# Performance work log

Measured on AMD Instinct MI355X. Metric: run time of the kernel, lower is better.

Reference implementation:

```python
import jax, jax.numpy as jnp
import numpy as np

B, L, D, H = 2, 2048, 1024, 16
HD = D // H


def setup_inputs() -> dict:
    key = jax.random.key(0)
    ks = jax.random.split(key, 14)
    s = 0.02
    return {
        "hidden_states": jax.random.normal(ks[0], (B, L, D), jnp.float32),
        "position_embeddings": jax.random.normal(ks[1], (B, L, D), jnp.float32),
        "Wcq": jax.random.normal(ks[2], (D, D), jnp.float32) * s,
        "bcq": jnp.zeros((D,), jnp.float32),
        "Wck": jax.random.normal(ks[3], (D, D), jnp.float32) * s,
        "bck": jnp.zeros((D,), jnp.float32),
        "Wpq": jax.random.normal(ks[4], (D, D), jnp.float32) * s,
        "bpq": jnp.zeros((D,), jnp.float32),
        "Wpk": jax.random.normal(ks[5], (D, D), jnp.float32) * s,
        "bpk": jnp.zeros((D,), jnp.float32),
        "rel_bias": jnp.zeros((1, H, 1, 1), jnp.float32),
        "Wo": jax.random.normal(ks[6], (D, D), jnp.float32) * s,
        "bo": jnp.zeros((D,), jnp.float32),
    }


def _split_heads(x):
    # [B, L, D] -> [B, H, L, HD]
    b, l, _ = x.shape
    return x.reshape(b, l, H, HD).transpose(0, 2, 1, 3)


def reference(hidden_states, position_embeddings, Wcq, bcq, Wck, bck,
              Wpq, bpq, Wpk, bpk, rel_bias, Wo, bo):
    cq = _split_heads(hidden_states @ Wcq + bcq)
    ck = _split_heads(hidden_states @ Wck + bck)
    # NOTE: original code (faithfully reproduced) uses content_key as the value
    cv = ck
    pq = _split_heads(position_embeddings @ Wpq + bpq)
    pk = _split_heads(position_embeddings @ Wpk + bpk)

    scores = (jnp.einsum("bhqd,bhkd->bhqk", cq, ck)
              + jnp.einsum("bhqd,bhkd->bhqk", pq, pk)
              + rel_bias)
    attn_weights = jax.nn.softmax(scores / jnp.sqrt(jnp.float32(HD)), axis=-1)
    ctx = jnp.einsum("bhqk,bhkd->bhqd", attn_weights, cv)
    ctx = ctx.transpose(0, 2, 1, 3).reshape(hidden_states.shape[0], -1, D)
    output = ctx @ Wo + bo
    return output, attn_weights
```

## Files before the change

kernel.cpp:

```cpp
#include <hip/hip_runtime.h>
#include <hip/hip_bf16.h>
#include <math.h>


#define Bc 2
#define Lc 2048
#define Dc 1024
#define Hc 16
#define Mc (Bc*Lc)
#define NT 32

typedef __attribute__((ext_vector_type(8))) __bf16 bf16x8;
typedef __attribute__((ext_vector_type(4))) float f32x4;
typedef __attribute__((ext_vector_type(16))) float f32x16;
typedef __attribute__((ext_vector_type(2))) unsigned u32x2;

union U4 { unsigned u[4]; bf16x8 v; };

__device__ __forceinline__ void gl_lds16(const void* g, void* l) {
    __builtin_amdgcn_global_load_lds(
        (const __attribute__((address_space(1))) void*)g,
        (__attribute__((address_space(3))) void*)l, 16, 0, 0);
}
__device__ __forceinline__ unsigned pkbf(float a, float b) {
    unsigned short ua = __builtin_bit_cast(unsigned short, (__bf16)a);
    unsigned short ub = __builtin_bit_cast(unsigned short, (__bf16)b);
    return (unsigned)ua | ((unsigned)ub << 16);
}
__device__ __forceinline__ float lo2f(unsigned u){ return __builtin_bit_cast(float, u << 16); }
__device__ __forceinline__ float hi2f(unsigned u){ return __builtin_bit_cast(float, u & 0xffff0000u); }
#define E2(x) __builtin_amdgcn_exp2f(x)

#define WAIT_VM0  asm volatile("s_waitcnt vmcnt(0)" ::: "memory")
#define WAIT_VM4  asm volatile("s_waitcnt vmcnt(4)" ::: "memory")
#define WAIT_VM8  asm volatile("s_waitcnt vmcnt(8)" ::: "memory")
#define WAIT_VM12 asm volatile("s_waitcnt vmcnt(12)" ::: "memory")
#define WAIT_LG0  asm volatile("s_waitcnt lgkmcnt(0)" ::: "memory")
#define SBAR __builtin_amdgcn_sched_barrier(0)
#define BARRIER do { __builtin_amdgcn_sched_barrier(0); __builtin_amdgcn_s_barrier(); __builtin_amdgcn_sched_barrier(0); } while (0)

__global__ __launch_bounds__(256) void prep_kernel(
    const float* __restrict__ hidden, const float* __restrict__ pos,
    const float* __restrict__ Wcq, const float* __restrict__ Wck,
    const float* __restrict__ Wpq, const float* __restrict__ Wpk,
    const float* __restrict__ Wo,
    __bf16* __restrict__ Wt, __bf16* __restrict__ Woh, __bf16* __restrict__ Wol,
    __bf16* __restrict__ Xh, __bf16* __restrict__ Xp)
{
    const int z = blockIdx.z;
    const int t = threadIdx.x;
    if (z >= 5) {
        const float* X = (z==5) ? hidden : pos;
        __bf16* dst    = (z==5) ? Xh : Xp;
        const size_t base = ((size_t)(blockIdx.y*16 + blockIdx.x)*256 + t) * 128;
        #pragma unroll
        for (int c = 0; c < 16; ++c) {
            const float* sp = X + base + c*8;
            float4 v0 = *(const float4*)sp;
            float4 v1 = *(const float4*)(sp + 4);
            bf16x8 o;
            o[0]=(__bf16)v0.x; o[1]=(__bf16)v0.y; o[2]=(__bf16)v0.z; o[3]=(__bf16)v0.w;
            o[4]=(__bf16)v1.x; o[5]=(__bf16)v1.y; o[6]=(__bf16)v1.z; o[7]=(__bf16)v1.w;
            *(bf16x8*)(dst + base + c*8) = o;
        }
        return;
    }
    const float* W = (z==0)?Wcq:(z==1)?Wck:(z==2)?Wpq:(z==3)?Wpk:Wo;
    const int n  = blockIdx.x*64 + (t & 63);
    const int k0 = blockIdx.y*128 + (t >> 6)*32;
    float v[32];
    #pragma unroll
    for (int j = 0; j < 32; ++j) v[j] = W[(size_t)(k0+j)*Dc + n];
    if (z < 4) {
        __bf16* dst = Wt + (size_t)z*Dc*Dc + (size_t)n*Dc + k0;
        #pragma unroll
        for (int c = 0; c < 4; ++c) {
            bf16x8 o;
            #pragma unroll
            for (int j = 0; j < 8; ++j) o[j] = (__bf16)v[c*8+j];
            *(bf16x8*)(dst + c*8) = o;
        }
    } else {
        __bf16* dh = Woh + (size_t)n*Dc + k0;
        __bf16* dl = Wol + (size_t)n*Dc + k0;
        #pragma unroll
        for (int c = 0; c < 4; ++c) {
            bf16x8 oh, ol;
            #pragma unroll
            for (int j = 0; j < 8; ++j) {
                float x = v[c*8+j];
                __bf16 hi = (__bf16)x;
                oh[j] = hi; ol[j] = (__bf16)(x - (float)hi);
            }
            *(bf16x8*)(dh + c*8) = oh;
            *(bf16x8*)(dl + c*8) = ol;
        }
    }
}

__global__ __launch_bounds__(256) void proj_kernel(
    const __bf16* __restrict__ Xh, const __bf16* __restrict__ Xp,
    const __bf16* __restrict__ Wt,
    const float* __restrict__ bcq, const float* __restrict__ bck,
    const float* __restrict__ bpq, const float* __restrict__ bpk,
    __bf16* __restrict__ Qc, __bf16* __restrict__ Kc)
{
    const int g = blockIdx.x;
    const int nblk = g >> 7, sg = g & 127, mblk = sg & 31, z = sg >> 5;
    const int m0 = mblk*128, n0 = nblk*128;
    const __bf16* X = (z < 2) ? Xh : Xp;
    const __bf16* Wz = Wt + (size_t)z*Dc*Dc;
    const float* bias = (z==0)?bcq:(z==1)?bck:(z==2)?bpq:bpk;
    __bf16* dst = (z & 1) ? Kc : Qc;
    const int half = z >> 1;
    const float scale = (z & 1) ? 1.0f : 0.18033688011112042f;

    const int t = threadIdx.x, lane = t & 63, w = t >> 6;
    const int wm = w >> 1, wn = w & 1;

    __shared__ __align__(16) __bf16 As[128][32];
    __shared__ __align__(16) __bf16 Bs[128][32];

    const int brow4 = lane >> 2;
    const int bcol  = ((lane & 3) ^ (brow4 & 3)) * 8;

    f32x4 acc[4][4] = {};

    for (int k0 = 0; k0 < Dc; k0 += 32) {
        #pragma unroll
        for (int i = 0; i < 2; ++i) {
            int row = 16*(2*w+i) + brow4;
            gl_lds16(X  + (size_t)(m0+row)*Dc + k0 + bcol, (char*)As + (2*w+i)*1024);
            gl_lds16(Wz + (size_t)(n0+row)*Dc + k0 + bcol, (char*)Bs + (2*w+i)*1024);
        }
        WAIT_VM0; __syncthreads();
        bf16x8 a[4], b[4];
        const int s2 = lane >> 4;
        #pragma unroll
        for (int i = 0; i < 4; ++i) {
            int Ra = wm*64 + i*16 + (lane&15);
            int Rb = wn*64 + i*16 + (lane&15);
            a[i] = *(const bf16x8*)((const char*)&As[Ra][0] + ((s2 ^ (Ra&3))*16));
            b[i] = *(const bf16x8*)((const char*)&Bs[Rb][0] + ((s2 ^ (Rb&3))*16));
        }
        #pragma unroll
        for (int mi = 0; mi < 4; ++mi)
            #pragma unroll
            for (int ni = 0; ni < 4; ++ni)
                acc[mi][ni] = __builtin_amdgcn_mfma_f32_16x16x32_bf16(a[mi], b[ni], acc[mi][ni], 0, 0, 0);
        __syncthreads();
    }
    #pragma unroll
    for (int mi = 0; mi < 4; ++mi)
        #pragma unroll
        for (int ni = 0; ni < 4; ++ni)
            #pragma unroll
            for (int r = 0; r < 4; ++r) {
                int row = m0 + wm*64 + mi*16 + (lane>>4)*4 + r;
                int col = n0 + wn*64 + ni*16 + (lane&15);
                float v = (acc[mi][ni][r] + bias[col]) * scale;
                int bb = row >> 11, l = row & (Lc-1);
                int hh = col >> 6,  hd = col & 63;
                dst[(((size_t)bb*Hc + hh)*Lc + l)*128 + half*64 + hd] = (__bf16)v;
            }
}

__global__ __launch_bounds__(256) void vt_kernel(
    const __bf16* __restrict__ Kc, __bf16* __restrict__ VT)
{
    const int l0 = blockIdx.x * 128, hb = blockIdx.y;
    const int t = threadIdx.x, w = t >> 6, lane = t & 63;
    __shared__ __bf16 T[128][72];
    const __bf16* src = Kc + ((size_t)hb*Lc + l0)*128;
    {
        const int lr = t >> 3, cc = t & 7;
        #pragma unroll
        for (int j = 0; j < 4; ++j)
            *(bf16x8*)&T[lr + j*32][cc*8] = *(const bf16x8*)(src + (size_t)(lr + j*32)*128 + cc*8);
    }
    __syncthreads();
    {
        const int d = lane;
        __bf16* dstp = VT + ((size_t)hb*64 + d)*Lc + l0 + w*32;
        #pragma unroll
        for (int j = 0; j < 4; ++j) {
            bf16x8 o;
            #pragma unroll
            for (int i = 0; i < 8; ++i) o[i] = T[w*32 + j*8 + i][d];
            *(bf16x8*)(dstp + j*8) = o;
        }
    }
}

__global__ __launch_bounds__(256, 3) void attn1_kernel(
    const __bf16* __restrict__ Qc, const __bf16* __restrict__ Kc,
    const float* __restrict__ rel_bias, float* __restrict__ baddp)
{
    const int g = blockIdx.x;
    const int qt = g >> 5, hb = g & 31, h = hb & 15;
    const int q0 = qt * 128;
    const int t = threadIdx.x, lane = t & 63, w = t >> 6;
    const int ln31 = lane & 31, hi = lane >> 5;

    const __bf16* Qp = Qc + (size_t)hb * Lc * 128;
    const __bf16* Kp = Kc + (size_t)hb * Lc * 128;

    __shared__ __align__(16) char smem[49152];

    bf16x8 qa[8];
    {
        const __bf16* qrow = Qp + (size_t)(q0 + w*32 + ln31) * 128 + hi*8;
        #pragma unroll
        for (int ks = 0; ks < 8; ++ks) qa[ks] = *(const bf16x8*)(qrow + ks*16);
    }

    int kof[4];
    #pragma unroll
    for (int c = 0; c < 4; ++c) {
        int rl = c*4 + (lane >> 4);
        int rr = w*16 + rl;
        kof[c] = rr*128 + (((lane & 15) ^ rl) * 8);
    }
    int kR[8];
    #pragma unroll
    for (int ks = 0; ks < 8; ++ks) kR[ks] = ((ks*2 + hi) ^ (lane & 15)) * 8;

    #define STAGE_K(B, KT) do { \
        const __bf16* kb_ = Kp + (size_t)(KT)*8192; \
        gl_lds16(kb_ + kof[0], smem + ((B)*64 + w*16 +  0)*256); \
        gl_lds16(kb_ + kof[1], smem + ((B)*64 + w*16 +  4)*256); \
        gl_lds16(kb_ + kof[2], smem + ((B)*64 + w*16 +  8)*256); \
        gl_lds16(kb_ + kof[3], smem + ((B)*64 + w*16 + 12)*256); \
    } while (0)
    #define KB(B, ROW, KS) (*(const bf16x8*)(smem + ((B)*64 + (ROW))*256 + kR[KS]*2))

    const float bc = rel_bias[h] * 0.18033688011112042f;
    float lp[4] = {0.f, 0.f, 0.f, 0.f};

    STAGE_K(0, 0); STAGE_K(1, 1);
    WAIT_VM4; BARRIER;
    for (int kt = 0; kt < NT; ++kt) {
        if (kt+2 < NT) STAGE_K((kt+2) % 3, kt+2);
        SBAR;
        const int buf = kt % 3;
        f32x16 s0, s1;
        #pragma unroll
        for (int r = 0; r < 16; ++r) { s0[r] = bc; s1[r] = bc; }
        __builtin_amdgcn_s_setprio(1);
        #pragma unroll
        for (int ks = 0; ks < 8; ++ks) {
            bf16x8 kb0 = KB(buf, ln31, ks);
            bf16x8 kb1 = KB(buf, 32 + ln31, ks);
            s0 = __builtin_amdgcn_mfma_f32_32x32x16_bf16(kb0, qa[ks], s0, 0, 0, 0);
            s1 = __builtin_amdgcn_mfma_f32_32x32x16_bf16(kb1, qa[ks], s1, 0, 0, 0);
        }
        __builtin_amdgcn_s_setprio(0);
        #pragma unroll
        for (int r = 0; r < 16; ++r) {
            lp[r & 3] += E2(s0[r]);
            lp[r & 3] += E2(s1[r]);
        }
        if (kt+2 < NT) { WAIT_VM4; } else { WAIT_VM0; }
        BARRIER;
    }
    float lsum = (lp[0] + lp[1]) + (lp[2] + lp[3]);
    lsum += __shfl_xor(lsum, 32);
    if (!hi) baddp[(size_t)hb*Lc + q0 + w*32 + ln31] = bc - log2f(lsum);
    #undef STAGE_K
    #undef KB
}

__global__ __launch_bounds__(256, 2) void attn2_kernel(
    const __bf16* __restrict__ Qc, const __bf16* __restrict__ Kc,
    const __bf16* __restrict__ VT, const float* __restrict__ baddp,
    float* __restrict__ attn, __bf16* __restrict__ ctxh)
{
    const int g = blockIdx.x;
    const int qt = g >> 5, hb = g & 31, h = hb & 15, bb = hb >> 4;
    const int q0 = qt * 128;
    const int t = threadIdx.x, lane = t & 63, w = t >> 6;
    const int ln31 = lane & 31, hi = lane >> 5;

    const __bf16* Qp = Qc + (size_t)hb * Lc * 128;
    const __bf16* Kp = Kc + (size_t)hb * Lc * 128;
    const __bf16* Vp = VT + (size_t)hb * 64 * Lc;

    __shared__ __align__(16) char smem[81920];
    char* const VsB = smem + 49152;
    char* const PsW = smem + 65536 + w*4096;

    bf16x8 qa[8];
    {
        const __bf16* qrow = Qp + (size_t)(q0 + w*32 + ln31) * 128 + hi*8;
        #pragma unroll
        for (int ks = 0; ks < 8; ++ks) qa[ks] = *(const bf16x8*)(qrow + ks*16);
    }
    const float badd = baddp[(size_t)hb*Lc + q0 + w*32 + ln31];

    int kof[4];
    #pragma unroll
    for (int c = 0; c < 4; ++c) {
        int rl = c*4 + (lane >> 4);
        int rr = w*16 + rl;
        kof[c] = rr*128 + (((lane & 15) ^ rl) * 8);
    }
    int vof[2];
    #pragma unroll
    for (int c = 0; c < 2; ++c) {
        int dl = lane >> 3;
        int dd = w*16 + c*8 + dl;
        vof[c] = dd*2048 + (((lane & 7) ^ dl) * 8);
    }
    int kR[8];
    #pragma unroll
    for (int ks = 0; ks < 8; ++ks) kR[ks] = ((ks*2 + hi) ^ (lane & 15)) * 8;
    int vR[4];
    #pragma unroll
    for (int ks = 0; ks < 4; ++ks) vR[ks] = ((ks*2 + hi) ^ (lane & 7)) * 8;

    #define STAGE_K(B, KT) do { \
        const __bf16* kb_ = Kp + (size_t)(KT)*8192; \
        gl_lds16(kb_ + kof[0], smem + ((B)*64 + w*16 +  0)*256); \
        gl_lds16(kb_ + kof[1], smem + ((B)*64 + w*16 +  4)*256); \
        gl_lds16(kb_ + kof[2], smem + ((B)*64 + w*16 +  8)*256); \
        gl_lds16(kb_ + kof[3], smem + ((B)*64 + w*16 + 12)*256); \
    } while (0)
    #define STAGE_V(B, KT) do { \
        const __bf16* vb_ = Vp + (KT)*64; \
        gl_lds16(vb_ + vof[0], VsB + ((B)*64 + w*16 + 0)*128); \
        gl_lds16(vb_ + vof[1], VsB + ((B)*64 + w*16 + 8)*128); \
    } while (0)
    #define KB(B, ROW, KS) (*(const bf16x8*)(smem + ((B)*64 + (ROW))*256 + kR[KS]*2))
    #define VB(B, ROW, KS) (*(const bf16x8*)(VsB  + ((B)*64 + (ROW))*128 + vR[KS]*2))

    f32x16 ctx0 = {}, ctx1 = {};
    float* abase = attn + ((size_t)hb*Lc + q0 + w*32)*Lc;
    const int rr2 = lane >> 4;
    const int s8  = lane & 15;

    STAGE_K(0, 0); STAGE_V(0, 0); STAGE_K(1, 1);
    WAIT_VM4; BARRIER;

    for (int kt = 0; kt < NT; ++kt) {
        if (kt+1 < NT) STAGE_V((kt+1) & 1, kt+1);
        if (kt+2 < NT) STAGE_K((kt+2) % 3, kt+2);
        SBAR;
        const int buf = kt % 3;
        f32x16 s0, s1;
        #pragma unroll
        for (int r = 0; r < 16; ++r) { s0[r] = badd; s1[r] = badd; }
        __builtin_amdgcn_s_setprio(1);
        #pragma unroll
        for (int ks = 0; ks < 8; ++ks) {
            bf16x8 kb0 = KB(buf, ln31, ks);
            bf16x8 kb1 = KB(buf, 32 + ln31, ks);
            s0 = __builtin_amdgcn_mfma_f32_32x32x16_bf16(kb0, qa[ks], s0, 0, 0, 0);
            s1 = __builtin_amdgcn_mfma_f32_32x32x16_bf16(kb1, qa[ks], s1, 0, 0, 0);
        }
        __builtin_amdgcn_s_setprio(0);
        unsigned u0[8], u1[8], r0[8], r1[8];
        #pragma unroll
        for (int gq = 0; gq < 4; ++gq) {
            u0[gq]   = pkbf(E2(s0[4*gq+0]), E2(s0[4*gq+1]));
            u1[gq]   = pkbf(E2(s0[4*gq+2]), E2(s0[4*gq+3]));
            u0[4+gq] = pkbf(E2(s1[4*gq+0]), E2(s1[4*gq+1]));
            u1[4+gq] = pkbf(E2(s1[4*gq+2]), E2(s1[4*gq+3]));
        }
        #pragma unroll
        for (int gq = 0; gq < 8; ++gq) {
            r0[gq] = __shfl_xor(u0[gq], 32);
            r1[gq] = __shfl_xor(u1[gq], 32);
        }
        bf16x8 pb[4];
        #pragma unroll
        for (int ks = 0; ks < 4; ++ks) {
            const int gq = 2*ks + hi;
            U4 u;
            u.u[0] = hi ? r0[gq] : u0[gq];
            u.u[1] = hi ? r1[gq] : u1[gq];
            u.u[2] = hi ? u0[gq] : r0[gq];
            u.u[3] = hi ? u1[gq] : r1[gq];
            pb[ks] = u.v;
            *(bf16x8*)(PsW + ln31*128 + ((gq ^ (ln31 & 7))*16)) = u.v;
        }
        __builtin_amdgcn_s_setprio(1);
        #pragma unroll
        for (int ks = 0; ks < 4; ++ks) {
            bf16x8 v0 = VB(kt & 1, ln31, ks);
            bf16x8 v1 = VB(kt & 1, 32 + ln31, ks);
            ctx0 = __builtin_amdgcn_mfma_f32_32x32x16_bf16(pb[ks], v0, ctx0, 0, 0, 0);
            ctx1 = __builtin_amdgcn_mfma_f32_32x32x16_bf16(pb[ks], v1, ctx1, 0, 0, 0);
        }
        __builtin_amdgcn_s_setprio(0);
        WAIT_LG0; SBAR;
        #pragma unroll
        for (int j = 0; j < 8; ++j) {
            const int row = j*4 + rr2;
            u32x2 d = *(const u32x2*)(PsW + row*128 + (((s8>>1) ^ (row&7))*16) + (s8&1)*8);
            f32x4 o;
            o[0]=lo2f(d[0]); o[1]=hi2f(d[0]); o[2]=lo2f(d[1]); o[3]=hi2f(d[1]);
            __builtin_nontemporal_store(o, (f32x4*)(abase + (size_t)row*Lc + kt*64 + s8*4));
        }
        if (kt+1 < NT) {
            if (kt+2 < NT) { WAIT_VM12; } else { WAIT_VM8; }
            BARRIER;
        }
    }

    #pragma unroll
    for (int r = 0; r < 16; ++r) {
        const int R = (r&3) + 8*(r>>2) + 4*hi;
        const size_t row = (size_t)bb*Lc + q0 + w*32 + R;
        ctxh[row*Dc + h*64 + ln31]      = (__bf16)ctx0[r];
        ctxh[row*Dc + h*64 + 32 + ln31] = (__bf16)ctx1[r];
    }
    #undef STAGE_K
    #undef STAGE_V
    #undef KB
    #undef VB
}

__global__ __launch_bounds__(256) void out_kernel(
    const __bf16* __restrict__ ctxh, const __bf16* __restrict__ Woh,
    const __bf16* __restrict__ Wol, const float* __restrict__ bo,
    float* __restrict__ out)
{
    const int m0 = blockIdx.y * 128, n0 = blockIdx.x * 128;
    const int t = threadIdx.x, lane = t & 63, w = t >> 6;
    const int wm = w >> 1, wn = w & 1;

    __shared__ __align__(16) __bf16 As[128][32];
    __shared__ __align__(16) __bf16 Bh[128][32];
    __shared__ __align__(16) __bf16 Bl[128][32];

    const int row4 = lane >> 2;
    const int scol = ((lane & 3) ^ (row4 & 3)) * 8;

    f32x4 acc[4][4] = {};

    for (int k0 = 0; k0 < Dc; k0 += 32) {
        #pragma unroll
        for (int i = 0; i < 2; ++i) {
            int row = 16*(2*w+i) + row4;
            gl_lds16(ctxh + (size_t)(m0+row)*Dc + k0 + scol, (char*)As + (2*w+i)*1024);
            gl_lds16(Woh  + (size_t)(n0+row)*Dc + k0 + scol, (char*)Bh + (2*w+i)*1024);
            gl_lds16(Wol  + (size_t)(n0+row)*Dc + k0 + scol, (char*)Bl + (2*w+i)*1024);
        }
        WAIT_VM0; __syncthreads();
        bf16x8 a[4], bh[4], bl[4];
        const int s2 = lane >> 4;
        #pragma unroll
        for (int i = 0; i < 4; ++i) {
            int Ra = wm*64 + i*16 + (lane&15);
            int Rb = wn*64 + i*16 + (lane&15);
            a[i]  = *(const bf16x8*)((const char*)&As[Ra][0] + ((s2 ^ (Ra&3))*16));
            bh[i] = *(const bf16x8*)((const char*)&Bh[Rb][0] + ((s2 ^ (Rb&3))*16));
            bl[i] = *(const bf16x8*)((const char*)&Bl[Rb][0] + ((s2 ^ (Rb&3))*16));
        }
        #pragma unroll
        for (int mi = 0; mi < 4; ++mi)
            #pragma unroll
            for (int ni = 0; ni < 4; ++ni) {
                acc[mi][ni] = __builtin_amdgcn_mfma_f32_16x16x32_bf16(a[mi], bh[ni], acc[mi][ni], 0, 0, 0);
                acc[mi][ni] = __builtin_amdgcn_mfma_f32_16x16x32_bf16(a[mi], bl[ni], acc[mi][ni], 0, 0, 0);
            }
        __syncthreads();
    }
    #pragma unroll
    for (int mi = 0; mi < 4; ++mi)
        #pragma unroll
        for (int ni = 0; ni < 4; ++ni)
            #pragma unroll
            for (int r = 0; r < 4; ++r) {
                int row = m0 + wm*64 + mi*16 + (lane>>4)*4 + r;
                int col = n0 + wn*64 + ni*16 + (lane&15);
                __builtin_nontemporal_store(acc[mi][ni][r] + bo[col],
                                            out + (size_t)row * Dc + col);
            }
}

extern "C" void kernel_launch(void* const* d_in, const int* in_sizes, int n_in,
                              void* d_out, int out_size, void* d_ws, size_t ws_size,
                              hipStream_t stream)
{
    const float* hidden = (const float*)d_in[0];
    const float* pos    = (const float*)d_in[1];
    const float* Wcq = (const float*)d_in[2];  const float* bcq = (const float*)d_in[3];
    const float* Wck = (const float*)d_in[4];  const float* bck = (const float*)d_in[5];
    const float* Wpq = (const float*)d_in[6];  const float* bpq = (const float*)d_in[7];
    const float* Wpk = (const float*)d_in[8];  const float* bpk = (const float*)d_in[9];
    const float* relb = (const float*)d_in[10];
    const float* Wo  = (const float*)d_in[11]; const float* bo  = (const float*)d_in[12];

    float* out  = (float*)d_out;
    float* attn = out + (size_t)Mc * Dc;

    __bf16* ws   = (__bf16*)d_ws;
    __bf16* Woh  = ws;
    __bf16* Wol  = ws + (1u<<20);
    __bf16* Wt   = ws + (2u<<20);
    __bf16* ctxh = Wt;
    __bf16* Qc   = ws + (6u<<20);
    __bf16* Kc   = ws + (14u<<20);
    __bf16* VTb  = ws + (22u<<20);
    float*  badd = (float*)(ws + (26u<<20));

    __bf16* Xh = (__bf16*)attn;
    __bf16* Xp = Xh + (4u<<20);

    prep_kernel<<<dim3(16, 8, 7), 256, 0, stream>>>(
        hidden, pos, Wcq, Wck, Wpq, Wpk, Wo, Wt, Woh, Wol, Xh, Xp);
    proj_kernel<<<dim3(1024), 256, 0, stream>>>(Xh, Xp, Wt, bcq, bck, bpq, bpk, Qc, Kc);
    vt_kernel<<<dim3(Lc/128, 32), 256, 0, stream>>>(Kc, VTb);
    attn1_kernel<<<dim3(512), 256, 0, stream>>>(Qc, Kc, relb, badd);
    attn2_kernel<<<dim3(512), 256, 0, stream>>>(Qc, Kc, VTb, badd, attn, ctxh);
    out_kernel<<<dim3(8, 32), 256, 0, stream>>>(ctxh, Woh, Wol, bo, out);
}
```

Before: 330.3 us.

## Triple-buffer LDS staging in projection and output GEMM kernels

The QK projection GEMM and the output GEMM move from a single shared-memory tile with a full load wait each k-step to a three-deep ring of buffers. Two stages are prefetched ahead, and partial vmcnt waits let global-to-LDS loads overlap the MFMA work. s_setprio is raised around the MFMA block so compute waves get scheduling priority. The cost is more LDS per block (48KB and 72KB), which may lower occupancy.

```diff
diff --git a/kernel.cpp b/kernel.cpp
--- a/kernel.cpp
+++ b/kernel.cpp
@@ -33,6 +33,7 @@
 
 #define WAIT_VM0  asm volatile("s_waitcnt vmcnt(0)" ::: "memory")
 #define WAIT_VM4  asm volatile("s_waitcnt vmcnt(4)" ::: "memory")
+#define WAIT_VM6  asm volatile("s_waitcnt vmcnt(6)" ::: "memory")
 #define WAIT_VM8  asm volatile("s_waitcnt vmcnt(8)" ::: "memory")
 #define WAIT_VM12 asm volatile("s_waitcnt vmcnt(12)" ::: "memory")
 #define WAIT_LG0  asm volatile("s_waitcnt lgkmcnt(0)" ::: "memory")
@@ -118,38 +119,49 @@
     const int t = threadIdx.x, lane = t & 63, w = t >> 6;
     const int wm = w >> 1, wn = w & 1;
 
-    __shared__ __align__(16) __bf16 As[128][32];
-    __shared__ __align__(16) __bf16 Bs[128][32];
+    __shared__ __align__(16) char smem[49152];
 
     const int brow4 = lane >> 2;
     const int bcol  = ((lane & 3) ^ (brow4 & 3)) * 8;
 
     f32x4 acc[4][4] = {};
 
-    for (int k0 = 0; k0 < Dc; k0 += 32) {
-        #pragma unroll
-        for (int i = 0; i < 2; ++i) {
-            int row = 16*(2*w+i) + brow4;
-            gl_lds16(X  + (size_t)(m0+row)*Dc + k0 + bcol, (char*)As + (2*w+i)*1024);
-            gl_lds16(Wz + (size_t)(n0+row)*Dc + k0 + bcol, (char*)Bs + (2*w+i)*1024);
-        }
-        WAIT_VM0; __syncthreads();
+    #define STAGE_P(B, KT) do { \
+        const int k0_ = (KT)*32; \
+        _Pragma("unroll") \
+        for (int i = 0; i < 2; ++i) { \
+            int row = 16*(2*w+i) + brow4; \
+            gl_lds16(X  + (size_t)(m0+row)*Dc + k0_ + bcol, smem + (B)*16384 + (2*w+i)*1024); \
+            gl_lds16(Wz + (size_t)(n0+row)*Dc + k0_ + bcol, smem + (B)*16384 + 8192 + (2*w+i)*1024); \
+        } \
+    } while (0)
+
+    STAGE_P(0, 0); STAGE_P(1, 1);
+    WAIT_VM4; BARRIER;
+    for (int kt = 0; kt < 32; ++kt) {
+        if (kt+2 < 32) STAGE_P((kt+2) % 3, kt+2);
+        SBAR;
+        const int buf = kt % 3;
         bf16x8 a[4], b[4];
         const int s2 = lane >> 4;
         #pragma unroll
         for (int i = 0; i < 4; ++i) {
             int Ra = wm*64 + i*16 + (lane&15);
             int Rb = wn*64 + i*16 + (lane&15);
-            a[i] = *(const bf16x8*)((const char*)&As[Ra][0] + ((s2 ^ (Ra&3))*16));
-            b[i] = *(const bf16x8*)((const char*)&Bs[Rb][0] + ((s2 ^ (Rb&3))*16));
-        }
+            a[i] = *(const bf16x8*)(smem + buf*16384 + Ra*64 + ((s2 ^ (Ra&3))*16));
+            b[i] = *(const bf16x8*)(smem + buf*16384 + 8192 + Rb*64 + ((s2 ^ (Rb&3))*16));
+        }
+        __builtin_amdgcn_s_setprio(1);
         #pragma unroll
         for (int mi = 0; mi < 4; ++mi)
             #pragma unroll
             for (int ni = 0; ni < 4; ++ni)
                 acc[mi][ni] = __builtin_amdgcn_mfma_f32_16x16x32_bf16(a[mi], b[ni], acc[mi][ni], 0, 0, 0);
-        __syncthreads();
-    }
+        __builtin_amdgcn_s_setprio(0);
+        if (kt+2 < 32) { WAIT_VM4; } else { WAIT_VM0; }
+        BARRIER;
+    }
+    #undef STAGE_P
     #pragma unroll
     for (int mi = 0; mi < 4; ++mi)
         #pragma unroll
@@ -429,34 +441,41 @@
     const int t = threadIdx.x, lane = t & 63, w = t >> 6;
     const int wm = w >> 1, wn = w & 1;
 
-    __shared__ __align__(16) __bf16 As[128][32];
-    __shared__ __align__(16) __bf16 Bh[128][32];
-    __shared__ __align__(16) __bf16 Bl[128][32];
+    __shared__ __align__(16) char smem[73728];
 
     const int row4 = lane >> 2;
     const int scol = ((lane & 3) ^ (row4 & 3)) * 8;
 
     f32x4 acc[4][4] = {};
 
-    for (int k0 = 0; k0 < Dc; k0 += 32) {
-        #pragma unroll
-        for (int i = 0; i < 2; ++i) {
-            int row = 16*(2*w+i) + row4;
-            gl_lds16(ctxh + (size_t)(m0+row)*Dc + k0 + scol, (char*)As + (2*w+i)*1024);
-            gl_lds16(Woh  + (size_t)(n0+row)*Dc + k0 + scol, (char*)Bh + (2*w+i)*1024);
-            gl_lds16(Wol  + (size_t)(n0+row)*Dc + k0 + scol, (char*)Bl + (2*w+i)*1024);
-        }
-        WAIT_VM0; __syncthreads();
+    #define STAGE_O(B, KT) do { \
+        const int k0_ = (KT)*32; \
+        _Pragma("unroll") \
+        for (int i = 0; i < 2; ++i) { \
+            int row = 16*(2*w+i) + row4; \
+            gl_lds16(ctxh + (size_t)(m0+row)*Dc + k0_ + scol, smem + (B)*24576 + (2*w+i)*1024); \
+            gl_lds16(Woh  + (size_t)(n0+row)*Dc + k0_ + scol, smem + (B)*24576 + 8192 + (2*w+i)*1024); \
+            gl_lds16(Wol  + (size_t)(n0+row)*Dc + k0_ + scol, smem + (B)*24576 + 16384 + (2*w+i)*1024); \
+        } \
+    } while (0)
+
+    STAGE_O(0, 0); STAGE_O(1, 1);
+    WAIT_VM6; BARRIER;
+    for (int kt = 0; kt < 32; ++kt) {
+        if (kt+2 < 32) STAGE_O((kt+2) % 3, kt+2);
+        SBAR;
+        const int buf = kt % 3;
         bf16x8 a[4], bh[4], bl[4];
         const int s2 = lane >> 4;
         #pragma unroll
         for (int i = 0; i < 4; ++i) {
             int Ra = wm*64 + i*16 + (lane&15);
             int Rb = wn*64 + i*16 + (lane&15);
-            a[i]  = *(const bf16x8*)((const char*)&As[Ra][0] + ((s2 ^ (Ra&3))*16));
-            bh[i] = *(const bf16x8*)((const char*)&Bh[Rb][0] + ((s2 ^ (Rb&3))*16));
-            bl[i] = *(const bf16x8*)((const char*)&Bl[Rb][0] + ((s2 ^ (Rb&3))*16));
-        }
+            a[i]  = *(const bf16x8*)(smem + buf*24576 + Ra*64 + ((s2 ^ (Ra&3))*16));
+            bh[i] = *(const bf16x8*)(smem + buf*24576 + 8192 + Rb*64 + ((s2 ^ (Rb&3))*16));
+            bl[i] = *(const bf16x8*)(smem + buf*24576 + 16384 + Rb*64 + ((s2 ^ (Rb&3))*16));
+        }
+        __builtin_amdgcn_s_setprio(1);
         #pragma unroll
         for (int mi = 0; mi < 4; ++mi)
             #pragma unroll
@@ -464,8 +483,11 @@
                 acc[mi][ni] = __builtin_amdgcn_mfma_f32_16x16x32_bf16(a[mi], bh[ni], acc[mi][ni], 0, 0, 0);
                 acc[mi][ni] = __builtin_amdgcn_mfma_f32_16x16x32_bf16(a[mi], bl[ni], acc[mi][ni], 0, 0, 0);
             }
-        __syncthreads();
-    }
+        __builtin_amdgcn_s_setprio(0);
+        if (kt+2 < 32) { WAIT_VM6; } else { WAIT_VM0; }
+        BARRIER;
+    }
+    #undef STAGE_O
     #pragma unroll
     for (int mi = 0; mi < 4; ++mi)
         #pragma unroll
```

Measured after the change: 310.1 us. -6.1%, faster.
